# Performance work log

Measured on AMD Instinct MI355X. Metric: run time of the kernel, lower is better.

The kernel has to match this reference:

```python
import jax, jax.numpy as jnp
import numpy as np

K, N, M, D, H = 3, 16384, 4096, 128, 64


def _phi(x, W1, b1, W2, b2, W3, b3):
    # x: [n, D]; weights stacked over kernels: W1 [K,H,D], W2/W3 [K,H,H], b* [K,H]
    h1 = jax.nn.softplus(jnp.einsum('nd,khd->knh', x, W1) + b1[:, None, :])
    h2 = jax.nn.softplus(jnp.einsum('knh,kgh->kng', h1, W2) + b2[:, None, :])
    return jnp.einsum('kng,kfg->knf', h2, W3) + b3[:, None, :]  # [K, n, H]


def setup_inputs() -> dict:
    key = jax.random.key(0)
    ks = jax.random.split(key, 10)
    s = lambda shp, fan: jax.random.normal(ks[0], shp)  # placeholder
    inp = {
        'x': jax.random.normal(ks[0], (N, D), jnp.float32),
        'z': jax.random.normal(ks[1], (M, D), jnp.float32),
        'W1': jax.random.normal(ks[2], (K, H, D), jnp.float32) / np.sqrt(H),
        'b1': jax.random.normal(ks[3], (K, H), jnp.float32) / np.sqrt(H),
        'W2': jax.random.normal(ks[4], (K, H, H), jnp.float32) / np.sqrt(H),
        'b2': jax.random.normal(ks[5], (K, H), jnp.float32) / np.sqrt(H),
        'W3': jax.random.normal(ks[6], (K, H, H), jnp.float32) / np.sqrt(H),
        'b3': jax.random.normal(ks[7], (K, H), jnp.float32) / np.sqrt(H),
        'log_sigma': jnp.array([0.0, 0.5185, 1.0], jnp.float32),
        'kernel_weights': jnp.zeros((K,), jnp.float32),
    }
    return inp


def reference(x, z, W1, b1, W2, b2, W3, b3, log_sigma, kernel_weights):
    fx = _phi(x, W1, b1, W2, b2, W3, b3)  # [K, N, H]
    fz = _phi(z, W1, b1, W2, b2, W3, b3)  # [K, M, H]
    # pairwise squared distance via expansion (same math as ((fx-fz)**2).sum(-1))
    sq = (jnp.sum(fx * fx, -1)[:, :, None]
          + jnp.sum(fz * fz, -1)[:, None, :]
          - 2.0 * jnp.einsum('knh,kmh->knm', fx, fz))  # [K, N, M]
    sq = jnp.maximum(sq, 0.0)
    inv2sig = 1.0 / (2.0 * jnp.power(10.0, log_sigma))  # [K]
    kxz = jnp.exp(-inv2sig[:, None, None] * sq)  # [K, N, M]
    w = jax.nn.softmax(kernel_weights)  # [K]
    return jnp.einsum('k,knm->nm', w, kxz)  # [N, M]
```

## Files before the change

kernel.cpp:

```cpp
#include <hip/hip_runtime.h>

typedef _Float16 half8 __attribute__((ext_vector_type(8)));
typedef float floatx4 __attribute__((ext_vector_type(4)));

#define K_ 3
#define N_ 16384
#define M_ 4096
#define D_ 128
#define H_ 64

#define OFF_FXH 0
#define SZ_FXH (K_*N_*H_*2)
#define OFF_FZH (OFF_FXH + SZ_FXH)
#define SZ_FZH (K_*M_*H_*2)
#define OFF_NXS (OFF_FZH + SZ_FZH)
#define SZ_NXS (K_*N_*4)
#define OFF_NZS (OFF_NXS + SZ_NXS)
#define SZ_NZS (K_*M_*4)
#define OFF_W1T (OFF_NZS + SZ_NZS)
#define SZ_W1T (K_*D_*H_*4)
#define OFF_W2T (OFF_W1T + SZ_W1T)
#define SZ_W2T (K_*H_*H_*4)
#define OFF_W3T (OFF_W2T + SZ_W2T)

__global__ void transpose_w(const float* __restrict__ W1,
                            const float* __restrict__ W2,
                            const float* __restrict__ W3,
                            float* __restrict__ W1t,
                            float* __restrict__ W2t,
                            float* __restrict__ W3t) {
  int idx = blockIdx.x * 256 + threadIdx.x;
  if (idx < K_*H_*D_) {
    int k = idx / (H_*D_); int r = idx % (H_*D_);
    int h = r / D_; int d = r % D_;
    W1t[k*(D_*H_) + d*H_ + h] = W1[idx];
  }
  if (idx < K_*H_*H_) {
    int k = idx / (H_*H_); int r = idx % (H_*H_);
    int g = r / H_; int h = r % H_;
    W2t[k*(H_*H_) + h*H_ + g] = W2[idx];
    W3t[k*(H_*H_) + h*H_ + g] = W3[idx];
  }
}

__device__ __forceinline__ float softplus_f(float x) {
  float p = exp2f(x * 1.44269504089f);
  float r = 0.693147180560f * log2f(1.0f + p);
  return (x > 20.0f) ? x : r;
}

__global__ __launch_bounds__(256) void phi_kernel(
    const float* __restrict__ x, const float* __restrict__ z,
    const float* __restrict__ W1t, const float* __restrict__ b1,
    const float* __restrict__ W2t, const float* __restrict__ b2,
    const float* __restrict__ W3t, const float* __restrict__ b3,
    const float* __restrict__ log_sigma,
    _Float16* __restrict__ fxh, float* __restrict__ nxs,
    _Float16* __restrict__ fzh, float* __restrict__ nzs)
{
  __shared__ float xbuf[64*132];
  __shared__ float hbuf[64*68];
  __shared__ float nred[64*4];

  const int which = blockIdx.z;
  const int nrows = which ? M_ : N_;
  if (blockIdx.x * 64 >= nrows) return;
  const float* __restrict__ src = which ? z : x;
  _Float16* __restrict__ dsth = which ? fzh : fxh;
  float* __restrict__ dstn = which ? nzs : nxs;

  const int t = threadIdx.x;
  const int lane = t & 63;
  const int wv = __builtin_amdgcn_readfirstlane(t >> 6);
  const int k = blockIdx.y;
  const int row0 = blockIdx.x * 64;
  const int row = row0 + lane;
  const int h0 = wv * 16;

  const float* __restrict__ w1 = W1t + k*(D_*H_);
  const float* __restrict__ w2 = W2t + k*(H_*H_);
  const float* __restrict__ w3 = W3t + k*(H_*H_);

  {
    const float4* __restrict__ gx = (const float4*)(src + (size_t)row0 * D_);
    #pragma unroll
    for (int it = 0; it < 8; it++) {
      int idx = t + it*256;
      int r = idx >> 5, c = idx & 31;
      *(float4*)&xbuf[r*132 + c*4] = gx[idx];
    }
  }
  __syncthreads();

  float acc[16];
  #pragma unroll
  for (int i=0;i<16;i++) acc[i] = b1[k*H_ + h0 + i];
  #pragma unroll 2
  for (int d4=0; d4<D_/4; d4++) {
    float4 xv = *(const float4*)&xbuf[lane*132 + d4*4];
    const float* wd = w1 + d4*4*H_ + h0;
    #pragma unroll
    for (int i=0;i<16;i++) acc[i] = fmaf(xv.x, wd[i], acc[i]);
    #pragma unroll
    for (int i=0;i<16;i++) acc[i] = fmaf(xv.y, wd[H_+i], acc[i]);
    #pragma unroll
    for (int i=0;i<16;i++) acc[i] = fmaf(xv.z, wd[2*H_+i], acc[i]);
    #pragma unroll
    for (int i=0;i<16;i++) acc[i] = fmaf(xv.w, wd[3*H_+i], acc[i]);
  }
  #pragma unroll
  for (int i=0;i<16;i+=4) {
    float4 v;
    v.x = softplus_f(acc[i+0]); v.y = softplus_f(acc[i+1]);
    v.z = softplus_f(acc[i+2]); v.w = softplus_f(acc[i+3]);
    *(float4*)&hbuf[lane*68 + h0 + i] = v;
  }
  __syncthreads();
  #pragma unroll
  for (int i=0;i<16;i++) acc[i] = b2[k*H_ + h0 + i];
  #pragma unroll 2
  for (int h4=0; h4<H_/4; h4++) {
    float4 hv = *(const float4*)&hbuf[lane*68 + h4*4];
    const float* wd = w2 + h4*4*H_ + h0;
    #pragma unroll
    for (int i=0;i<16;i++) acc[i] = fmaf(hv.x, wd[i], acc[i]);
    #pragma unroll
    for (int i=0;i<16;i++) acc[i] = fmaf(hv.y, wd[H_+i], acc[i]);
    #pragma unroll
    for (int i=0;i<16;i++) acc[i] = fmaf(hv.z, wd[2*H_+i], acc[i]);
    #pragma unroll
    for (int i=0;i<16;i++) acc[i] = fmaf(hv.w, wd[3*H_+i], acc[i]);
  }
  __syncthreads();
  #pragma unroll
  for (int i=0;i<16;i+=4) {
    float4 v;
    v.x = softplus_f(acc[i+0]); v.y = softplus_f(acc[i+1]);
    v.z = softplus_f(acc[i+2]); v.w = softplus_f(acc[i+3]);
    *(float4*)&hbuf[lane*68 + h0 + i] = v;
  }
  __syncthreads();
  #pragma unroll
  for (int i=0;i<16;i++) acc[i] = b3[k*H_ + h0 + i];
  #pragma unroll 2
  for (int h4=0; h4<H_/4; h4++) {
    float4 hv = *(const float4*)&hbuf[lane*68 + h4*4];
    const float* wd = w3 + h4*4*H_ + h0;
    #pragma unroll
    for (int i=0;i<16;i++) acc[i] = fmaf(hv.x, wd[i], acc[i]);
    #pragma unroll
    for (int i=0;i<16;i++) acc[i] = fmaf(hv.y, wd[H_+i], acc[i]);
    #pragma unroll
    for (int i=0;i<16;i++) acc[i] = fmaf(hv.z, wd[2*H_+i], acc[i]);
    #pragma unroll
    for (int i=0;i<16;i++) acc[i] = fmaf(hv.w, wd[3*H_+i], acc[i]);
  }
  float lsv = log_sigma[k];
  float inv2sig = 0.5f * exp2f(-lsv * 3.32192809489f);
  float c2 = inv2sig * 1.44269504089f;
  float s = sqrtf(c2);
  half8 u0, u1;
  float nsum = 0.f;
  #pragma unroll
  for (int i=0;i<8;i++) {
    _Float16 v = (_Float16)(s * acc[i]);
    u0[i] = v; float f = (float)v; nsum = fmaf(f, f, nsum);
  }
  #pragma unroll
  for (int i=0;i<8;i++) {
    _Float16 v = (_Float16)(s * acc[8+i]);
    u1[i] = v; float f = (float)v; nsum = fmaf(f, f, nsum);
  }
  _Float16* dp = dsth + ((size_t)k*nrows + row)*H_ + h0;
  *(half8*)dp = u0;
  *(half8*)(dp + 8) = u1;
  nred[lane*4 + wv] = nsum;
  __syncthreads();
  if (t < 64) {
    float v = nred[t*4+0] + nred[t*4+1] + nred[t*4+2] + nred[t*4+3];
    dstn[(size_t)k*nrows + row] = v;
  }
}

__global__ __launch_bounds__(512, 4) void dkef_main(
    const _Float16* __restrict__ fxh, const _Float16* __restrict__ fzh,
    const float* __restrict__ nxs, const float* __restrict__ nzs,
    const float* __restrict__ kw, float* __restrict__ out)
{
  __shared__ __align__(16) _Float16 Ab[128*72];
  __shared__ __align__(16) _Float16 Bb[128*72];
  __shared__ float nxl[128];
  __shared__ float nzl[128];

  const int t = threadIdx.x;
  const int lane = t & 63;
  const int wv = t >> 6;

  const int NTM = M_/128;
  const int orig = blockIdx.y * NTM + blockIdx.x;
  const int swz = (orig & 7) * ((NTM*(N_/128)) >> 3) + (orig >> 3);
  const int m0 = (swz % NTM) * 128;
  const int n0 = (swz / NTM) * 128;

  float k0 = kw[0], k1 = kw[1], k2 = kw[2];
  float mx = fmaxf(k0, fmaxf(k1, k2));
  float e0 = exp2f((k0 - mx) * 1.44269504089f);
  float e1 = exp2f((k1 - mx) * 1.44269504089f);
  float e2 = exp2f((k2 - mx) * 1.44269504089f);
  float winv = 1.0f / (e0 + e1 + e2);
  float wk3[3] = {e0 * winv, e1 * winv, e2 * winv};

  const int wa = (wv >> 2) * 64;
  const int wb = (wv & 3) * 32;
  const int fr = lane & 15;
  const int fq = lane >> 4;

  floatx4 oacc[4][2] = {};

  for (int k = 0; k < K_; k++) {
    __syncthreads();
    {
      const int4* ga = (const int4*)(fxh + ((size_t)k*N_ + n0)*H_);
      #pragma unroll
      for (int it = 0; it < 2; it++) {
        int idx = t + it*512;
        int r = idx >> 3, c = idx & 7;
        *(int4*)&Ab[r*72 + c*8] = ga[idx];
      }
      const int4* gb = (const int4*)(fzh + ((size_t)k*M_ + m0)*H_);
      #pragma unroll
      for (int it = 0; it < 2; it++) {
        int idx = t + it*512;
        int r = idx >> 3, c = idx & 7;
        *(int4*)&Bb[r*72 + c*8] = gb[idx];
      }
      if (t < 128) nxl[t] = nxs[(size_t)k*N_ + n0 + t];
      else if (t < 256) nzl[t-128] = nzs[(size_t)k*M_ + m0 + (t-128)];
    }
    __syncthreads();

    floatx4 dacc[4][2] = {};
    #pragma unroll
    for (int ks = 0; ks < 2; ks++) {
      half8 af[4], bf[2];
      #pragma unroll
      for (int i = 0; i < 4; i++)
        af[i] = *(const half8*)&Ab[(wa + i*16 + fr)*72 + ks*32 + fq*8];
      #pragma unroll
      for (int j = 0; j < 2; j++)
        bf[j] = *(const half8*)&Bb[(wb + j*16 + fr)*72 + ks*32 + fq*8];
      #pragma unroll
      for (int i = 0; i < 4; i++)
        #pragma unroll
        for (int j = 0; j < 2; j++)
          dacc[i][j] = __builtin_amdgcn_mfma_f32_16x16x32_f16(af[i], bf[j], dacc[i][j], 0, 0, 0);
    }

    float wkv = wk3[k];
    #pragma unroll
    for (int i = 0; i < 4; i++) {
      floatx4 nx4 = *(const floatx4*)&nxl[wa + i*16 + fq*4];
      #pragma unroll
      for (int j = 0; j < 2; j++) {
        float nzv = nzl[wb + j*16 + fr];
        #pragma unroll
        for (int r = 0; r < 4; r++) {
          float sm = nx4[r] + nzv;
          float e = fmaf(2.0f, dacc[i][j][r], -sm);
          e = fminf(e, 0.0f);
          oacc[i][j][r] = fmaf(wkv, exp2f(e), oacc[i][j][r]);
        }
      }
    }
  }

  #pragma unroll
  for (int i = 0; i < 4; i++) {
    #pragma unroll
    for (int r = 0; r < 4; r++) {
      size_t rowg = (size_t)(n0 + wa + i*16 + fq*4 + r);
      float* orow = out + rowg * M_ + m0 + wb + fr;
      #pragma unroll
      for (int j = 0; j < 2; j++)
        __builtin_nontemporal_store(oacc[i][j][r], &orow[j*16]);
    }
  }
}

extern "C" void kernel_launch(void* const* d_in, const int* in_sizes, int n_in,
                              void* d_out, int out_size, void* d_ws, size_t ws_size,
                              hipStream_t stream) {
  const float* x  = (const float*)d_in[0];
  const float* z  = (const float*)d_in[1];
  const float* W1 = (const float*)d_in[2];
  const float* b1 = (const float*)d_in[3];
  const float* W2 = (const float*)d_in[4];
  const float* b2 = (const float*)d_in[5];
  const float* W3 = (const float*)d_in[6];
  const float* b3 = (const float*)d_in[7];
  const float* ls = (const float*)d_in[8];
  const float* kw = (const float*)d_in[9];
  float* out = (float*)d_out;

  char* ws = (char*)d_ws;
  _Float16* fxh = (_Float16*)(ws + OFF_FXH);
  _Float16* fzh = (_Float16*)(ws + OFF_FZH);
  float* nxs = (float*)(ws + OFF_NXS);
  float* nzs = (float*)(ws + OFF_NZS);
  float* W1t = (float*)(ws + OFF_W1T);
  float* W2t = (float*)(ws + OFF_W2T);
  float* W3t = (float*)(ws + OFF_W3T);

  hipLaunchKernelGGL(transpose_w, dim3((K_*H_*D_ + 255)/256), dim3(256), 0, stream,
                     W1, W2, W3, W1t, W2t, W3t);
  hipLaunchKernelGGL(phi_kernel, dim3(N_/64, K_, 2), dim3(256), 0, stream,
                     x, z, W1t, b1, W2t, b2, W3t, b3, ls, fxh, nxs, fzh, nzs);
  hipLaunchKernelGGL(dkef_main, dim3(M_/128, N_/128), dim3(512), 0, stream,
                     fxh, fzh, nxs, nzs, kw, out);
}
```

Measured before the change: 376.7 us.

## Store features in MFMA fragment order and load operands directly from global memory

phi_kernel now writes the fp16 features in a layout that matches the MFMA 16x16x32 fragment arrangement. dkef_main can then read A and B fragments straight from global memory with coalesced 16-byte loads, which removes the LDS staging and both __syncthreads per kernel. The main kernel also goes from 512 to 256 threads per block, with each wave computing a 64x64 tile (4x4 fragments) instead of 64x32. This raises register use and relies on L1/L2 reuse in place of shared memory, which could reduce occupancy.

```diff
diff --git a/kernel.cpp b/kernel.cpp
--- a/kernel.cpp
+++ b/kernel.cpp
@@ -23,6 +23,7 @@
 #define SZ_W2T (K_*H_*H_*4)
 #define OFF_W3T (OFF_W2T + SZ_W2T)
 
+
 __global__ void transpose_w(const float* __restrict__ W1,
                             const float* __restrict__ W2,
                             const float* __restrict__ W3,
@@ -171,9 +172,16 @@
     _Float16 v = (_Float16)(s * acc[8+i]);
     u1[i] = v; float f = (float)v; nsum = fmaf(f, f, nsum);
   }
-  _Float16* dp = dsth + ((size_t)k*nrows + row)*H_ + h0;
-  *(half8*)dp = u0;
-  *(half8*)(dp + 8) = u1;
+  {
+    const int c16 = row >> 4;
+    const int frp = row & 15;
+    const int ks0 = wv >> 1;
+    const int fq0 = (wv & 1) * 2;
+    _Float16* dp = dsth + ((size_t)(k*(nrows >> 4) + c16))*1024
+                        + ks0*512 + fq0*128 + frp*8;
+    *(half8*)dp = u0;
+    *(half8*)(dp + 128) = u1;
+  }
   nred[lane*4 + wv] = nsum;
   __syncthreads();
   if (t < 64) {
@@ -182,16 +190,11 @@
   }
 }
 
-__global__ __launch_bounds__(512, 4) void dkef_main(
+__global__ __launch_bounds__(256, 3) void dkef_main(
     const _Float16* __restrict__ fxh, const _Float16* __restrict__ fzh,
     const float* __restrict__ nxs, const float* __restrict__ nzs,
     const float* __restrict__ kw, float* __restrict__ out)
 {
-  __shared__ __align__(16) _Float16 Ab[128*72];
-  __shared__ __align__(16) _Float16 Bb[128*72];
-  __shared__ float nxl[128];
-  __shared__ float nzl[128];
-
   const int t = threadIdx.x;
   const int lane = t & 63;
   const int wv = t >> 6;
@@ -210,63 +213,48 @@
   float winv = 1.0f / (e0 + e1 + e2);
   float wk3[3] = {e0 * winv, e1 * winv, e2 * winv};
 
-  const int wa = (wv >> 2) * 64;
-  const int wb = (wv & 3) * 32;
+  const int wa = (wv >> 1) * 64;
+  const int wb = (wv & 1) * 64;
   const int fr = lane & 15;
   const int fq = lane >> 4;
 
-  floatx4 oacc[4][2] = {};
+  floatx4 oacc[4][4] = {};
+
+  const int cn = (n0 + wa) >> 4;
+  const int cm = (m0 + wb) >> 4;
 
   for (int k = 0; k < K_; k++) {
-    __syncthreads();
-    {
-      const int4* ga = (const int4*)(fxh + ((size_t)k*N_ + n0)*H_);
+    const _Float16* pa = fxh + ((size_t)(k*(N_/16) + cn))*1024 + fq*128 + fr*8;
+    const _Float16* pb = fzh + ((size_t)(k*(M_/16) + cm))*1024 + fq*128 + fr*8;
+    half8 bf[4][2];
+    #pragma unroll
+    for (int j = 0; j < 4; j++) {
+      bf[j][0] = *(const half8*)(pb + j*1024);
+      bf[j][1] = *(const half8*)(pb + j*1024 + 512);
+    }
+    floatx4 nx4[4];
+    float nzv[4];
+    #pragma unroll
+    for (int i = 0; i < 4; i++)
+      nx4[i] = *(const floatx4*)&nxs[(size_t)k*N_ + n0 + wa + i*16 + fq*4];
+    #pragma unroll
+    for (int j = 0; j < 4; j++)
+      nzv[j] = nzs[(size_t)k*M_ + m0 + wb + j*16 + fr];
+
+    float wkv = wk3[k];
+    #pragma unroll
+    for (int i = 0; i < 4; i++) {
+      half8 a0 = *(const half8*)(pa + i*1024);
+      half8 a1 = *(const half8*)(pa + i*1024 + 512);
       #pragma unroll
-      for (int it = 0; it < 2; it++) {
-        int idx = t + it*512;
-        int r = idx >> 3, c = idx & 7;
-        *(int4*)&Ab[r*72 + c*8] = ga[idx];
-      }
-      const int4* gb = (const int4*)(fzh + ((size_t)k*M_ + m0)*H_);
-      #pragma unroll
-      for (int it = 0; it < 2; it++) {
-        int idx = t + it*512;
-        int r = idx >> 3, c = idx & 7;
-        *(int4*)&Bb[r*72 + c*8] = gb[idx];
-      }
-      if (t < 128) nxl[t] = nxs[(size_t)k*N_ + n0 + t];
-      else if (t < 256) nzl[t-128] = nzs[(size_t)k*M_ + m0 + (t-128)];
-    }
-    __syncthreads();
-
-    floatx4 dacc[4][2] = {};
-    #pragma unroll
-    for (int ks = 0; ks < 2; ks++) {
-      half8 af[4], bf[2];
-      #pragma unroll
-      for (int i = 0; i < 4; i++)
-        af[i] = *(const half8*)&Ab[(wa + i*16 + fr)*72 + ks*32 + fq*8];
-      #pragma unroll
-      for (int j = 0; j < 2; j++)
-        bf[j] = *(const half8*)&Bb[(wb + j*16 + fr)*72 + ks*32 + fq*8];
-      #pragma unroll
-      for (int i = 0; i < 4; i++)
-        #pragma unroll
-        for (int j = 0; j < 2; j++)
-          dacc[i][j] = __builtin_amdgcn_mfma_f32_16x16x32_f16(af[i], bf[j], dacc[i][j], 0, 0, 0);
-    }
-
-    float wkv = wk3[k];
-    #pragma unroll
-    for (int i = 0; i < 4; i++) {
-      floatx4 nx4 = *(const floatx4*)&nxl[wa + i*16 + fq*4];
-      #pragma unroll
-      for (int j = 0; j < 2; j++) {
-        float nzv = nzl[wb + j*16 + fr];
+      for (int j = 0; j < 4; j++) {
+        floatx4 d = {};
+        d = __builtin_amdgcn_mfma_f32_16x16x32_f16(a0, bf[j][0], d, 0, 0, 0);
+        d = __builtin_amdgcn_mfma_f32_16x16x32_f16(a1, bf[j][1], d, 0, 0, 0);
         #pragma unroll
         for (int r = 0; r < 4; r++) {
-          float sm = nx4[r] + nzv;
-          float e = fmaf(2.0f, dacc[i][j][r], -sm);
+          float sm = nx4[i][r] + nzv[j];
+          float e = fmaf(2.0f, d[r], -sm);
           e = fminf(e, 0.0f);
           oacc[i][j][r] = fmaf(wkv, exp2f(e), oacc[i][j][r]);
         }
@@ -281,7 +269,7 @@
       size_t rowg = (size_t)(n0 + wa + i*16 + fq*4 + r);
       float* orow = out + rowg * M_ + m0 + wb + fr;
       #pragma unroll
-      for (int j = 0; j < 2; j++)
+      for (int j = 0; j < 4; j++)
         __builtin_nontemporal_store(oacc[i][j][r], &orow[j*16]);
     }
   }
@@ -315,6 +303,6 @@
                      W1, W2, W3, W1t, W2t, W3t);
   hipLaunchKernelGGL(phi_kernel, dim3(N_/64, K_, 2), dim3(256), 0, stream,
                      x, z, W1t, b1, W2t, b2, W3t, b3, ls, fxh, nxs, fzh, nzs);
-  hipLaunchKernelGGL(dkef_main, dim3(M_/128, N_/128), dim3(512), 0, stream,
+  hipLaunchKernelGGL(dkef_main, dim3(M_/128, N_/128), dim3(256), 0, stream,
                      fxh, fzh, nxs, nzs, kw, out);
 }
```

Result: faster. 357.7 us (-5.0%).
